# Optimization experiments

Measured on AMD Instinct MI355X. Metric: run time of the kernel, lower is better.

The kernel has to match this reference:

```python
import jax, jax.numpy as jnp
import numpy as np

B, C, H, W = 4, 256, 96, 96
HEADS, RATE = 8, 1


def setup_inputs() -> dict:
    key = jax.random.key(0)
    ks = [jax.random.fold_in(key, i) for i in range(8)]
    kpe = 2 * (RATE // 2) + 1  # PE depthwise kernel size (1 for rate=1)
    return {
        "q": jax.random.normal(ks[0], (B, C, H, W), jnp.float32),
        "k": jax.random.normal(ks[1], (B, C, H, W), jnp.float32),
        "v": jax.random.normal(ks[2], (B, C, H, W), jnp.float32),
        "wq": jax.random.normal(ks[3], (C, C), jnp.float32) * 0.02,          # q_proj 1x1 (used for q,k,v per source)
        "pe_dw": jax.random.normal(ks[4], (9, 1, kpe, kpe), jnp.float32) * 0.3,  # grouped conv, groups=9
        "pe_pw": jax.random.normal(ks[5], (9, 9, 1, 1), jnp.float32) * 0.3,      # 1x1 mixing conv
        "wo": jax.random.normal(ks[6], (C, C), jnp.float32) * 0.02,          # out_proj weight
        "bo": jax.random.normal(ks[7], (C,), jnp.float32) * 0.02,            # out_proj bias
    }


def _unfold3(x, rate):
    # torch.nn.Unfold(3, dilation=rate, padding=rate) then view(N, c, 9, H, W)
    # kernel positions are row-major (ki, kj), channel-major layout -> stack on axis 2.
    n, c, h, w = x.shape
    xp = jnp.pad(x, ((0, 0), (0, 0), (rate, rate), (rate, rate)))
    pats = [xp[:, :, i * rate:i * rate + h, j * rate:j * rate + w]
            for i in range(3) for j in range(3)]
    return jnp.stack(pats, axis=2)  # (N, c, 9, H, W)


def reference(q, b_unused_k=None, v=None, wq=None, pe_dw=None, pe_pw=None, wo=None, bo=None, k=None):
    raise NotImplementedError  # replaced below


def reference(q, k, v, wq, pe_dw, pe_pw, wo, bo):
    b = q.shape[0]
    ch = C // HEADS
    proj = lambda x: jnp.einsum('oc,bchw->bohw', wq, x)  # source uses q_proj for q, k AND v
    qh = proj(q).reshape(b * HEADS, ch, H, W)
    kh = proj(k).reshape(b * HEADS, ch, H, W)
    vh = proj(v).reshape(b * HEADS, ch, H, W)

    ku = _unfold3(kh, RATE)                              # (bH, ch, 9, H, W)
    f = jnp.einsum('nchw,nckhw->nkhw', qh, ku)           # per-pixel 3x3 scores (bH, 9, H, W)

    pad = RATE // 2
    dn = ('NCHW', 'OIHW', 'NCHW')
    f = jax.lax.conv_general_dilated(f, pe_dw, (1, 1), [(pad, pad), (pad, pad)],
                                     feature_group_count=9, dimension_numbers=dn)
    f = jax.lax.conv_general_dilated(f, pe_pw, (1, 1), 'VALID', dimension_numbers=dn)
    s = jax.nn.softmax(f, axis=1)                        # softmax over 9 kernel positions

    vu = _unfold3(vh, RATE)                              # (bH, ch, 9, H, W)
    o = jnp.einsum('nckhw,nkhw->nchw', vu, s).reshape(b, C, H, W)
    return jnp.einsum('oc,bchw->bohw', wo, o) + bo[None, :, None, None]
```

## Files before the change

kernel.cpp:

```cpp
#include <hip/hip_runtime.h>
#include <math.h>

#define HH 96
#define WW 96
#define PP 9216
#define CCH 256
#define BB 4
#define CH 32

typedef unsigned short u16;
typedef short bf16x8 __attribute__((ext_vector_type(8)));
typedef float f32x4 __attribute__((ext_vector_type(4)));

__device__ __forceinline__ float bf2f(unsigned s) { return __uint_as_float(s << 16); }
__device__ __forceinline__ u16 f2bf(float f) {
  unsigned u = __float_as_uint(f);
  return (u16)((u + 0x7fffu + ((u >> 16) & 1u)) >> 16);
}

typedef __attribute__((address_space(1))) const unsigned int GUI;
typedef __attribute__((address_space(3))) unsigned int LUI;
__device__ __forceinline__ void gload16(const void* g, void* l) {
  __builtin_amdgcn_global_load_lds((GUI*)g, (LUI*)l, 16, 0, 0);
}

__global__ __launch_bounds__(256)
void wcvt(const float* __restrict__ wq, const float* __restrict__ wo,
          u16* __restrict__ Wbf) {
  int gidx = blockIdx.x * 256 + threadIdx.x;
  int mat = gidx >> 13;
  int gi = gidx & 8191;
  int l = gi & 63;
  int i = (gi >> 6) & 3;
  int w = (gi >> 8) & 3;
  int ks = (gi >> 10) & 1;
  int kk = (gi >> 11) & 3;
  const float* W = mat ? wo : wq;
  int row = w * 64 + i * 16 + (l & 15);
  int c0 = kk * 64 + (ks * 4 + (l >> 4)) * 8;
  const float* s = W + (size_t)row * CCH + c0;
  float4 a = *(const float4*)s;
  float4 b = *(const float4*)(s + 4);
  uint4 u;
  u.x = (unsigned)f2bf(a.x) | ((unsigned)f2bf(a.y) << 16);
  u.y = (unsigned)f2bf(a.z) | ((unsigned)f2bf(a.w) << 16);
  u.z = (unsigned)f2bf(b.x) | ((unsigned)f2bf(b.y) << 16);
  u.w = (unsigned)f2bf(b.z) | ((unsigned)f2bf(b.w) << 16);
  *(uint4*)(Wbf + (size_t)gidx * 8) = u;
}

#define XROW 264
__global__ __launch_bounds__(256)
void gemm_qkvf(const float* __restrict__ qin, const float* __restrict__ kin,
               const float* __restrict__ vin, const u16* __restrict__ Wbf,
               u16* __restrict__ Xcl) {
  __shared__ u16 Xb[64 * XROW];
  const int t = threadIdx.x;
  const int w = t >> 6, l = t & 63;
  const int lr = l & 15, lg = l >> 4;
  const int pblk = blockIdx.x * 64;
  const int z = blockIdx.z;
  const int b = z & 3, which = z >> 2;
  const float* Xf = ((which == 0) ? qin : (which == 1) ? kin : vin) + (size_t)b * CCH * PP;
  u16* Y = Xcl + (size_t)z * ((size_t)PP * CCH);

  float4 xr[16];
#pragma unroll
  for (int rr = 0; rr < 16; rr++) {
    int cc = w * 64 + rr * 4 + lg;
    xr[rr] = *(const float4*)(Xf + (size_t)cc * PP + pblk + lr * 4);
  }
#pragma unroll
  for (int rr = 0; rr < 16; rr++) {
    float r0 = xr[rr].x, r1 = xr[rr].y, r2 = xr[rr].z, r3 = xr[rr].w;
    bool b0 = (lg & 1), b1 = (lg & 2);
    float s0 = b0 ? r0 : r1;
    float s1 = b0 ? r2 : r3;
    float u0 = __shfl_xor(s0, 16, 64);
    float u1 = __shfl_xor(s1, 16, 64);
    float m0 = b0 ? u0 : r0;
    float m1 = b0 ? r1 : u0;
    float m2 = b0 ? u1 : r2;
    float m3 = b0 ? r3 : u1;
    float s2 = b1 ? m0 : m2;
    float s3 = b1 ? m1 : m3;
    float w0 = __shfl_xor(s2, 32, 64);
    float w1 = __shfl_xor(s3, 32, 64);
    float o0 = b1 ? w0 : m0;
    float o1 = b1 ? w1 : m1;
    float o2 = b1 ? m2 : w0;
    float o3 = b1 ? m3 : w1;
    int cbase = w * 64 + rr * 4;
    int pl = lr * 4 + lg;
    unsigned lo = (unsigned)f2bf(o0) | ((unsigned)f2bf(o1) << 16);
    unsigned hi = (unsigned)f2bf(o2) | ((unsigned)f2bf(o3) << 16);
    *(uint2*)(&Xb[pl * XROW + cbase]) = make_uint2(lo, hi);
  }
  __syncthreads();

  f32x4 acc[4][4];
#pragma unroll
  for (int mi = 0; mi < 4; mi++)
#pragma unroll
    for (int ni = 0; ni < 4; ni++) acc[mi][ni] = (f32x4){0.f, 0.f, 0.f, 0.f};

#pragma unroll
  for (int kk = 0; kk < 4; kk++)
#pragma unroll
    for (int ks = 0; ks < 2; ks++) {
      const int q = kk * 8 + ks * 4 + lg;
      bf16x8 wf[4], xf[4];
#pragma unroll
      for (int i = 0; i < 4; i++) {
        size_t go = ((((size_t)(kk * 2 + ks) * 4 + w) * 4 + i) * 64 + l) * 8;
        wf[i] = *(const bf16x8*)(Wbf + go);
      }
#pragma unroll
      for (int i = 0; i < 4; i++) {
        int row = i * 16 + lr;
        xf[i] = *(const bf16x8*)&Xb[row * XROW + q * 8];
      }
#pragma unroll
      for (int mi = 0; mi < 4; mi++)
#pragma unroll
        for (int ni = 0; ni < 4; ni++)
          acc[mi][ni] = __builtin_amdgcn_mfma_f32_16x16x32_bf16(
              wf[mi], xf[ni], acc[mi][ni], 0, 0, 0);
    }

#pragma unroll
  for (int mi = 0; mi < 4; mi++)
#pragma unroll
    for (int ni = 0; ni < 4; ni++) {
      int o = w * 64 + mi * 16 + lg * 4;
      int p = pblk + ni * 16 + lr;
      f32x4 a = acc[mi][ni];
      uint2 u;
      u.x = (unsigned)f2bf(a[0]) | ((unsigned)f2bf(a[1]) << 16);
      u.y = (unsigned)f2bf(a[2]) | ((unsigned)f2bf(a[3]) << 16);
      *(uint2*)(Y + (size_t)p * CCH + o) = u;
    }
}

__global__ __launch_bounds__(256)
void gemm_out_m(const u16* __restrict__ Xbuf, const u16* __restrict__ Wbf,
                const float* __restrict__ bias, float* __restrict__ outY) {
  __shared__ u16 Xl[64 * 256];
  const int t = threadIdx.x;
  const int w = t >> 6, l = t & 63;
  const int lr = l & 15, lg = l >> 4;
  const int pblk = blockIdx.x * 64;
  const int z = blockIdx.z;
  const u16* Xb = Xbuf + (size_t)z * ((size_t)PP * CCH);

#pragma unroll
  for (int r = 0; r < 8; r++) {
    int G = r * 256 + t;
    int row = G >> 5, g = G & 31;
    int gs = (g & 24) | ((g & 7) ^ (row & 7));
    gload16(Xb + (size_t)(pblk + row) * CCH + gs * 8, (void*)&Xl[(size_t)G * 8]);
  }
  __syncthreads();

  f32x4 acc[4][4];
#pragma unroll
  for (int mi = 0; mi < 4; mi++)
#pragma unroll
    for (int ni = 0; ni < 4; ni++) acc[mi][ni] = (f32x4){0.f, 0.f, 0.f, 0.f};

#pragma unroll
  for (int kk = 0; kk < 4; kk++)
#pragma unroll
    for (int ks = 0; ks < 2; ks++) {
      const int q = kk * 8 + ks * 4 + lg;
      bf16x8 wf[4], xf[4];
#pragma unroll
      for (int i = 0; i < 4; i++) {
        size_t go = ((((size_t)(kk * 2 + ks) * 4 + w) * 4 + i) * 64 + l) * 8;
        wf[i] = *(const bf16x8*)(Wbf + go);
      }
#pragma unroll
      for (int i = 0; i < 4; i++) {
        int row = i * 16 + lr;
        int qp = (q & 24) | ((q & 7) ^ (row & 7));
        xf[i] = *(const bf16x8*)&Xl[row * 256 + qp * 8];
      }
#pragma unroll
      for (int mi = 0; mi < 4; mi++)
#pragma unroll
        for (int ni = 0; ni < 4; ni++)
          acc[mi][ni] = __builtin_amdgcn_mfma_f32_16x16x32_bf16(
              xf[mi], wf[ni], acc[mi][ni], 0, 0, 0);
    }

#pragma unroll
  for (int ni = 0; ni < 4; ni++) {
    int o = w * 64 + ni * 16 + lr;
    float bv = bias[o];
#pragma unroll
    for (int mi = 0; mi < 4; mi++) {
      int p = pblk + mi * 16 + lg * 4;
      f32x4 a = acc[mi][ni];
      float4 st = {a[0] + bv, a[1] + bv, a[2] + bv, a[3] + bv};
      *(float4*)(outY + ((size_t)z * CCH + o) * PP + p) = st;
    }
  }
}

#define TX 32
#define TY 4
#define HX 34
#define HY 6
#define NHP (HX * HY)
#define NGR (NHP * 4)
#define ARND 4

__device__ __forceinline__ void fma8(const uint4 u, const float* qp, float& s) {
  s = fmaf(qp[0], bf2f(u.x & 0xffffu), s);
  s = fmaf(qp[1], bf2f(u.x >> 16), s);
  s = fmaf(qp[2], bf2f(u.y & 0xffffu), s);
  s = fmaf(qp[3], bf2f(u.y >> 16), s);
  s = fmaf(qp[4], bf2f(u.z & 0xffffu), s);
  s = fmaf(qp[5], bf2f(u.z >> 16), s);
  s = fmaf(qp[6], bf2f(u.w & 0xffffu), s);
  s = fmaf(qp[7], bf2f(u.w >> 16), s);
}
__device__ __forceinline__ void acc8(const uint4 u, float gv, float* op) {
  op[0] = fmaf(gv, bf2f(u.x & 0xffffu), op[0]);
  op[1] = fmaf(gv, bf2f(u.x >> 16), op[1]);
  op[2] = fmaf(gv, bf2f(u.y & 0xffffu), op[2]);
  op[3] = fmaf(gv, bf2f(u.y >> 16), op[3]);
  op[4] = fmaf(gv, bf2f(u.z & 0xffffu), op[4]);
  op[5] = fmaf(gv, bf2f(u.z >> 16), op[5]);
  op[6] = fmaf(gv, bf2f(u.w & 0xffffu), op[6]);
  op[7] = fmaf(gv, bf2f(u.w >> 16), op[7]);
}

__global__ __launch_bounds__(256)
void attn_1b(const u16* __restrict__ Kt, const u16* __restrict__ Vt,
             u16* __restrict__ Qt, const float* __restrict__ pe_dw,
             const float* __restrict__ pe_pw) {
  __shared__ __align__(16) u16 kl[NHP * 32];
  __shared__ __align__(16) u16 vl[NHP * 32];
  __shared__ float coef[81];
  const int t = threadIdx.x;
  if (t < 81) coef[t] = pe_pw[t] * pe_dw[t % 9];

  const int lx = t & 31;
  const int h2 = (t >> 5) & 1;
  const int ly = t >> 6;
  const int x0 = blockIdx.x * TX;
  const int y0 = blockIdx.y * TY;
  const int b = blockIdx.z >> 3;
  const int h = blockIdx.z & 7;
  const size_t nbase = (size_t)b * PP * CCH + h * CH;
  const int p = (y0 + ly) * WW + (x0 + lx);
  const size_t pixhalf = nbase + (size_t)p * CCH + h2 * 16;

  uint4 kg[ARND], vg[ARND];
#pragma unroll
  for (int r = 0; r < ARND; r++) {
    int s = t + r * 256;
    int pix = s >> 2, g = s & 3;
    int hy = pix / HX, hx = pix - hy * HX;
    int gx = x0 - 1 + hx, gy = y0 - 1 + hy;
    bool ok = (s < NGR) & (gx >= 0) & (gx < WW) & (gy >= 0) & (gy < HH);
    uint4 u = make_uint4(0u, 0u, 0u, 0u);
    if (ok) u = *(const uint4*)(Kt + nbase + (size_t)(gy * WW + gx) * CCH + g * 8);
    kg[r] = u;
  }
#pragma unroll
  for (int r = 0; r < ARND; r++) {
    int s = t + r * 256;
    int pix = s >> 2, g = s & 3;
    int hy = pix / HX, hx = pix - hy * HX;
    int gx = x0 - 1 + hx, gy = y0 - 1 + hy;
    bool ok = (s < NGR) & (gx >= 0) & (gx < WW) & (gy >= 0) & (gy < HH);
    uint4 u = make_uint4(0u, 0u, 0u, 0u);
    if (ok) u = *(const uint4*)(Vt + nbase + (size_t)(gy * WW + gx) * CCH + g * 8);
    vg[r] = u;
  }
  uint4 q0 = *(const uint4*)(Qt + pixhalf);
  uint4 q1 = *(const uint4*)(Qt + pixhalf + 8);

#pragma unroll
  for (int r = 0; r < ARND; r++) {
    int s = t + r * 256;
    if (s < NGR) {
      int pix = s >> 2, g = s & 3;
      *(uint4*)(&kl[pix * 32 + (((g + (pix >> 1)) & 3) << 3)]) = kg[r];
    }
  }
#pragma unroll
  for (int r = 0; r < ARND; r++) {
    int s = t + r * 256;
    if (s < NGR) {
      int pix = s >> 2, g = s & 3;
      *(uint4*)(&vl[pix * 32 + (((g + (pix >> 1)) & 3) << 3)]) = vg[r];
    }
  }
  __syncthreads();

  float qh[16];
  qh[0] = bf2f(q0.x & 0xffffu); qh[1] = bf2f(q0.x >> 16);
  qh[2] = bf2f(q0.y & 0xffffu); qh[3] = bf2f(q0.y >> 16);
  qh[4] = bf2f(q0.z & 0xffffu); qh[5] = bf2f(q0.z >> 16);
  qh[6] = bf2f(q0.w & 0xffffu); qh[7] = bf2f(q0.w >> 16);
  qh[8] = bf2f(q1.x & 0xffffu); qh[9] = bf2f(q1.x >> 16);
  qh[10] = bf2f(q1.y & 0xffffu); qh[11] = bf2f(q1.y >> 16);
  qh[12] = bf2f(q1.z & 0xffffu); qh[13] = bf2f(q1.z >> 16);
  qh[14] = bf2f(q1.w & 0xffffu); qh[15] = bf2f(q1.w >> 16);

  float f[9];
#pragma unroll
  for (int kk = 0; kk < 9; kk++) {
    int pix = (ly + kk / 3) * HX + lx + kk % 3;
    int ga = h2 * 2;
    uint4 ka = *(const uint4*)(&kl[pix * 32 + (((ga + (pix >> 1)) & 3) << 3)]);
    uint4 kb = *(const uint4*)(&kl[pix * 32 + (((ga + 1 + (pix >> 1)) & 3) << 3)]);
    float s = 0.f;
    fma8(ka, qh, s);
    fma8(kb, qh + 8, s);
    f[kk] = s + __shfl_xor(s, 32, 64);
  }

  float g[9], m = -1e30f;
#pragma unroll
  for (int k2 = 0; k2 < 9; k2++) {
    float s = 0.f;
#pragma unroll
    for (int kk = 0; kk < 9; kk++) s = fmaf(coef[k2 * 9 + kk], f[kk], s);
    g[k2] = s;
    m = fmaxf(m, s);
  }
  float ssum = 0.f;
#pragma unroll
  for (int k2 = 0; k2 < 9; k2++) {
    g[k2] = __expf(g[k2] - m);
    ssum += g[k2];
  }
  float inv = 1.f / ssum;
#pragma unroll
  for (int k2 = 0; k2 < 9; k2++) g[k2] *= inv;

  float oh[16];
#pragma unroll
  for (int j = 0; j < 16; j++) oh[j] = 0.f;
#pragma unroll
  for (int kk = 0; kk < 9; kk++) {
    int pix = (ly + kk / 3) * HX + lx + kk % 3;
    int ga = h2 * 2;
    uint4 va = *(const uint4*)(&vl[pix * 32 + (((ga + (pix >> 1)) & 3) << 3)]);
    uint4 vb = *(const uint4*)(&vl[pix * 32 + (((ga + 1 + (pix >> 1)) & 3) << 3)]);
    acc8(va, g[kk], oh);
    acc8(vb, g[kk], oh + 8);
  }
  uint4 s0, s1;
  s0.x = (unsigned)f2bf(oh[0]) | ((unsigned)f2bf(oh[1]) << 16);
  s0.y = (unsigned)f2bf(oh[2]) | ((unsigned)f2bf(oh[3]) << 16);
  s0.z = (unsigned)f2bf(oh[4]) | ((unsigned)f2bf(oh[5]) << 16);
  s0.w = (unsigned)f2bf(oh[6]) | ((unsigned)f2bf(oh[7]) << 16);
  s1.x = (unsigned)f2bf(oh[8]) | ((unsigned)f2bf(oh[9]) << 16);
  s1.y = (unsigned)f2bf(oh[10]) | ((unsigned)f2bf(oh[11]) << 16);
  s1.z = (unsigned)f2bf(oh[12]) | ((unsigned)f2bf(oh[13]) << 16);
  s1.w = (unsigned)f2bf(oh[14]) | ((unsigned)f2bf(oh[15]) << 16);
  *(uint4*)(Qt + pixhalf) = s0;
  *(uint4*)(Qt + pixhalf + 8) = s1;
}

extern "C" void kernel_launch(void* const* d_in, const int* in_sizes, int n_in,
                              void* d_out, int out_size, void* d_ws, size_t ws_size,
                              hipStream_t stream) {
  const float* q     = (const float*)d_in[0];
  const float* k     = (const float*)d_in[1];
  const float* v     = (const float*)d_in[2];
  const float* wq    = (const float*)d_in[3];
  const float* pe_dw = (const float*)d_in[4];
  const float* pe_pw = (const float*)d_in[5];
  const float* wo    = (const float*)d_in[6];
  const float* bo    = (const float*)d_in[7];
  float* out = (float*)d_out;

  const size_t seg = (size_t)BB * PP * CCH;
  u16* Xcl = (u16*)d_ws;
  u16* Wbf = Xcl + 3 * seg;

  wcvt<<<64, 256, 0, stream>>>(wq, wo, Wbf);

  gemm_qkvf<<<dim3(PP / 64, 1, 12), 256, 0, stream>>>(q, k, v, Wbf, Xcl);

  u16* Qs = Xcl;
  u16* Ks = Xcl + seg;
  u16* Vs = Xcl + 2 * seg;
  attn_1b<<<dim3(WW / TX, HH / TY, BB * 8), 256, 0, stream>>>(Ks, Vs, Qs, pe_dw, pe_pw);

  gemm_out_m<<<dim3(PP / 64, 1, BB), 256, 0, stream>>>(Qs, Wbf + 65536, bo, out);
}
```

Before: 90.43 us.

## Split fused fp32 load+projection into transpose prepass and LDS-swizzled bf16 GEMM

```diff
diff --git a/kernel.cpp b/kernel.cpp
--- a/kernel.cpp
+++ b/kernel.cpp
@@ -49,52 +49,59 @@
   *(uint4*)(Wbf + (size_t)gidx * 8) = u;
 }
 
-#define XROW 264
 __global__ __launch_bounds__(256)
-void gemm_qkvf(const float* __restrict__ qin, const float* __restrict__ kin,
-               const float* __restrict__ vin, const u16* __restrict__ Wbf,
-               u16* __restrict__ Xcl) {
-  __shared__ u16 Xb[64 * XROW];
+void prepass(const float* __restrict__ q, const float* __restrict__ k,
+             const float* __restrict__ v, u16* __restrict__ Xcl) {
+  __shared__ float Tt[64][33];
+  const int t = threadIdx.x;
+  const int pblk = blockIdx.x * 64;
+  const int c0 = blockIdx.y * 32;
+  const int b = blockIdx.z & 3;
+  const int which = blockIdx.z >> 2;
+  const float* X = ((which == 0) ? q : (which == 1) ? k : v) + (size_t)b * CCH * PP;
+  u16* Y = Xcl + (size_t)blockIdx.z * ((size_t)PP * CCH);
+
+  {
+    int p4 = t & 15, c = t >> 4;
+#pragma unroll
+    for (int i = 0; i < 2; i++) {
+      int cc = c + 16 * i;
+      float4 vv = *(const float4*)(X + (size_t)(c0 + cc) * PP + pblk + p4 * 4);
+      Tt[p4 * 4 + 0][cc] = vv.x;
+      Tt[p4 * 4 + 1][cc] = vv.y;
+      Tt[p4 * 4 + 2][cc] = vv.z;
+      Tt[p4 * 4 + 3][cc] = vv.w;
+    }
+  }
+  __syncthreads();
+  int p = t >> 2, cg = t & 3;
+  unsigned wds[4];
+#pragma unroll
+  for (int j = 0; j < 4; j++) {
+    u16 lo = f2bf(Tt[p][cg * 8 + 2 * j]);
+    u16 hi = f2bf(Tt[p][cg * 8 + 2 * j + 1]);
+    wds[j] = (unsigned)lo | ((unsigned)hi << 16);
+  }
+  uint4 st = {wds[0], wds[1], wds[2], wds[3]};
+  *(uint4*)(Y + (size_t)(pblk + p) * CCH + c0 + cg * 8) = st;
+}
+
+__global__ __launch_bounds__(256)
+void gemm_proj(u16* __restrict__ Xcl, const u16* __restrict__ Wbf) {
+  __shared__ u16 Xl[64 * 256];
   const int t = threadIdx.x;
   const int w = t >> 6, l = t & 63;
   const int lr = l & 15, lg = l >> 4;
   const int pblk = blockIdx.x * 64;
   const int z = blockIdx.z;
-  const int b = z & 3, which = z >> 2;
-  const float* Xf = ((which == 0) ? qin : (which == 1) ? kin : vin) + (size_t)b * CCH * PP;
-  u16* Y = Xcl + (size_t)z * ((size_t)PP * CCH);
-
-  float4 xr[16];
-#pragma unroll
-  for (int rr = 0; rr < 16; rr++) {
-    int cc = w * 64 + rr * 4 + lg;
-    xr[rr] = *(const float4*)(Xf + (size_t)cc * PP + pblk + lr * 4);
-  }
-#pragma unroll
-  for (int rr = 0; rr < 16; rr++) {
-    float r0 = xr[rr].x, r1 = xr[rr].y, r2 = xr[rr].z, r3 = xr[rr].w;
-    bool b0 = (lg & 1), b1 = (lg & 2);
-    float s0 = b0 ? r0 : r1;
-    float s1 = b0 ? r2 : r3;
-    float u0 = __shfl_xor(s0, 16, 64);
-    float u1 = __shfl_xor(s1, 16, 64);
-    float m0 = b0 ? u0 : r0;
-    float m1 = b0 ? r1 : u0;
-    float m2 = b0 ? u1 : r2;
-    float m3 = b0 ? r3 : u1;
-    float s2 = b1 ? m0 : m2;
-    float s3 = b1 ? m1 : m3;
-    float w0 = __shfl_xor(s2, 32, 64);
-    float w1 = __shfl_xor(s3, 32, 64);
-    float o0 = b1 ? w0 : m0;
-    float o1 = b1 ? w1 : m1;
-    float o2 = b1 ? m2 : w0;
-    float o3 = b1 ? m3 : w1;
-    int cbase = w * 64 + rr * 4;
-    int pl = lr * 4 + lg;
-    unsigned lo = (unsigned)f2bf(o0) | ((unsigned)f2bf(o1) << 16);
-    unsigned hi = (unsigned)f2bf(o2) | ((unsigned)f2bf(o3) << 16);
-    *(uint2*)(&Xb[pl * XROW + cbase]) = make_uint2(lo, hi);
+  u16* Xb = Xcl + (size_t)z * ((size_t)PP * CCH);
+
+#pragma unroll
+  for (int r = 0; r < 8; r++) {
+    int G = r * 256 + t;
+    int row = G >> 5, g = G & 31;
+    int gs = (g & 24) | ((g & 7) ^ (row & 7));
+    gload16(Xb + (size_t)(pblk + row) * CCH + gs * 8, (void*)&Xl[(size_t)G * 8]);
   }
   __syncthreads();
 
@@ -118,7 +125,8 @@
 #pragma unroll
       for (int i = 0; i < 4; i++) {
         int row = i * 16 + lr;
-        xf[i] = *(const bf16x8*)&Xb[row * XROW + q * 8];
+        int qp = (q & 24) | ((q & 7) ^ (row & 7));
+        xf[i] = *(const bf16x8*)&Xl[row * 256 + qp * 8];
       }
 #pragma unroll
       for (int mi = 0; mi < 4; mi++)
@@ -138,7 +146,7 @@
       uint2 u;
       u.x = (unsigned)f2bf(a[0]) | ((unsigned)f2bf(a[1]) << 16);
       u.y = (unsigned)f2bf(a[2]) | ((unsigned)f2bf(a[3]) << 16);
-      *(uint2*)(Y + (size_t)p * CCH + o) = u;
+      *(uint2*)(Xb + (size_t)p * CCH + o) = u;
     }
 }
 
@@ -387,7 +395,9 @@
 
   wcvt<<<64, 256, 0, stream>>>(wq, wo, Wbf);
 
-  gemm_qkvf<<<dim3(PP / 64, 1, 12), 256, 0, stream>>>(q, k, v, Wbf, Xcl);
+  prepass<<<dim3(PP / 64, CCH / 32, 12), 256, 0, stream>>>(q, k, v, Xcl);
+
+  gemm_proj<<<dim3(PP / 64, 1, 12), 256, 0, stream>>>(Xcl, Wbf);
 
   u16* Qs = Xcl;
   u16* Ks = Xcl + seg;
```

Result: slower. 103.8 us (+14.8%).
